# Kernel optimization log

Hardware: AMD Instinct MI355X
Metric: run time of the kernel (lower is better)

Reference implementation:

```python
import jax, jax.numpy as jnp
import numpy as np
from jax import lax

EPS = 1e-8

def _norm(v, eps=EPS):
    # matches torch F.normalize: v / max(||v||, eps)
    return v / jnp.maximum(jnp.linalg.norm(v, axis=-1, keepdims=True), eps)

def keep_r6(r6):
    v1 = _norm(r6[..., :3])
    v2 = r6[..., 3:6]
    v2 = v2 - jnp.sum(v2 * v1, axis=-1, keepdims=True) * v1
    v2n = jnp.linalg.norm(v2, axis=-1, keepdims=True)
    mask = (v2n < 1e-6).astype(r6.dtype)
    e1 = jnp.array([1.0, 0.0, 0.0], dtype=r6.dtype)
    e2 = jnp.array([0.0, 1.0, 0.0], dtype=r6.dtype)
    dot = jnp.abs(jnp.sum(v1 * e1, axis=-1, keepdims=True))
    fb = jnp.where(dot < 0.9, e1, e2)
    fb_v2 = jnp.cross(v1, jnp.broadcast_to(fb, v1.shape), axis=-1)
    v2 = (1.0 - mask) * v2 + mask * fb_v2
    v2 = _norm(v2)
    return jnp.concatenate([v1, v2], axis=-1)

def r6_to_matrix(r6):
    r6 = keep_r6(r6)
    v1, v2 = r6[..., :3], r6[..., 3:6]
    v3 = jnp.cross(v1, v2, axis=-1)
    R = jnp.stack([v1, v2, v3], axis=-1)  # columns v1,v2,v3
    det = jnp.linalg.det(R)
    return R * jnp.sign(det)[..., None, None]

def instance_norm(x, eps=1e-5):
    # InstanceNorm3d, affine=False: per-(B,C) stats over spatial dims, biased var
    mu = jnp.mean(x, axis=(2, 3, 4), keepdims=True)
    var = jnp.mean((x - mu) ** 2, axis=(2, 3, 4), keepdims=True)
    return (x - mu) * lax.rsqrt(var + eps)

def conv1x1(x, w, b):
    return jnp.einsum('oc,bcdhw->bodhw', w[:, :, 0, 0, 0], x) + b[None, :, None, None, None]

def conv3_circ(x, w, b):
    xp = jnp.pad(x, ((0, 0), (0, 0), (1, 1), (1, 1), (1, 1)), mode='wrap')
    out = lax.conv_general_dilated(xp, w, (1, 1, 1), 'VALID',
                                   dimension_numbers=('NCDHW', 'OIDHW', 'NCDHW'))
    return out + b[None, :, None, None, None]

def _gelu(t):
    return jax.nn.gelu(t, approximate=False)

def _forward(x, pos_emb, qkv_w, qkv_b, lp1_w, lp1_b, lp2_w, lp2_b,
             mod1_w, mod1_b, mod2_w, mod2_b, pa_w, pa_b,
             R6_d, R6_h, R6_w, proj_w, proj_b):
    B, C, D, H, W = x.shape
    NH = pa_w.shape[0]
    HD = C // NH
    NV = HD // 3
    scale = HD ** (-0.5)

    # PositionalProcessing (deterministic; computed once, reused for all 3 axes)
    local = conv1x1(_gelu(instance_norm(conv3_circ(pos_emb, lp1_w, lp1_b))), lp2_w, lp2_b)
    mod = jax.nn.sigmoid(conv1x1(_gelu(instance_norm(conv1x1(local, mod1_w, mod1_b))), mod2_w, mod2_b))
    x_mod = x * mod
    pos_attn = _gelu(instance_norm(conv1x1(pos_emb, pa_w, pa_b)))  # [B,NH,D,H,W]

    axes = [
        (R6_d, (0, 3, 4, 1, 2), (0, 4, 3, 1, 2)),  # depth
        (R6_h, (0, 2, 4, 1, 3), (0, 4, 1, 3, 2)),  # height
        (R6_w, (0, 2, 3, 1, 4), (0, 4, 1, 2, 3)),  # width
    ]
    out_sum = 0.0
    for R6, perm, inv in axes:
        xp = jnp.transpose(x_mod, perm)      # [B, A1, A2, C, L]
        Bb, A1, A2, _, L = xp.shape
        bd = Bb * A1 * A2
        xl = jnp.swapaxes(xp.reshape(bd, C, L), -1, -2)  # [bd, L, C]
        qkv = (xl @ qkv_w.T + qkv_b).reshape(bd, L, 3, NH, HD)
        qkv = jnp.transpose(qkv, (2, 0, 3, 1, 4))
        q, k, v = qkv[0], qkv[1], qkv[2]     # [bd, NH, L, HD]
        R = r6_to_matrix(keep_r6(R6))[0]     # [NH, 3, 3]

        def rot(t):
            tv = t.reshape(bd, NH, L, NV, 3)
            return jnp.einsum('hij,bhlvj->bhlvi', R, tv).reshape(bd, NH, L, HD)

        attn = jnp.einsum('bhqd,bhkd->bhqk', rot(q), rot(k)) * scale
        pa = jnp.transpose(pos_attn, perm).reshape(bd, NH, L)
        attn = jax.nn.softmax(attn + pa[..., None], axis=-1)
        o = jnp.einsum('bhqk,bhkd->bhqd', attn, v)      # [bd, NH, L, HD]
        o = jnp.swapaxes(o, 1, 2).reshape(Bb, A1, A2, L, C)
        out_sum = out_sum + jnp.transpose(o, inv)        # [B, C, D, H, W]
    return conv1x1(out_sum, proj_w, proj_b)


def setup_inputs() -> dict:
    key = jax.random.key(0)
    ks = jax.random.split(key, 20)
    B, C, D, H, W, NH = 2, 96, 40, 40, 40, 4

    def rn(k, shape, s=0.05):
        return jax.random.normal(k, shape, dtype=jnp.float32) * s

    return {
        'x': jax.random.normal(ks[0], (B, C, D, H, W), dtype=jnp.float32),
        'pos_emb': jax.random.normal(ks[1], (B, C, D, H, W), dtype=jnp.float32),
        'qkv_w': rn(ks[2], (3 * C, C)), 'qkv_b': rn(ks[3], (3 * C,)),
        'lp1_w': rn(ks[4], (C, C, 3, 3, 3)), 'lp1_b': rn(ks[5], (C,)),
        'lp2_w': rn(ks[6], (C, C, 1, 1, 1)), 'lp2_b': rn(ks[7], (C,)),
        'mod1_w': rn(ks[8], (C, C, 1, 1, 1)), 'mod1_b': rn(ks[9], (C,)),
        'mod2_w': rn(ks[10], (C, C, 1, 1, 1)), 'mod2_b': rn(ks[11], (C,)),
        'pa_w': rn(ks[12], (NH, C, 1, 1, 1)), 'pa_b': rn(ks[13], (NH,)),
        'R6_d': jax.random.normal(ks[14], (1, NH, 6), dtype=jnp.float32),
        'R6_h': jax.random.normal(ks[15], (1, NH, 6), dtype=jnp.float32),
        'R6_w': jax.random.normal(ks[16], (1, NH, 6), dtype=jnp.float32),
        'proj_w': rn(ks[17], (C, C, 1, 1, 1)), 'proj_b': rn(ks[18], (C,)),
    }


def reference(x, pos_emb, qkv_w, qkv_b, lp1_w, lp1_b, lp2_w, lp2_b,
              mod1_w, mod1_b, mod2_w, mod2_b, pa_w, pa_b,
              R6_d, R6_h, R6_w, proj_w, proj_b):
    return _forward(x, pos_emb, qkv_w, qkv_b, lp1_w, lp1_b, lp2_w, lp2_b,
                    mod1_w, mod1_b, mod2_w, mod2_b, pa_w, pa_b,
                    R6_d, R6_h, R6_w, proj_w, proj_b)
```

## Files before the change

### kernel.cpp

```cpp
#include <hip/hip_runtime.h>


typedef __attribute__((ext_vector_type(8))) _Float16 half8;
typedef __attribute__((ext_vector_type(2))) _Float16 half2;
typedef __attribute__((ext_vector_type(16))) float floatx16;

static __device__ __forceinline__ half2 h2(unsigned int u) {
    return __builtin_bit_cast(half2, u);
}
static __device__ __forceinline__ float fdot2(unsigned int a, unsigned int b, float c) {
    return __builtin_amdgcn_fdot2(h2(a), h2(b), c, false);
}

__global__ void k_zero(float* __restrict__ p) {
    int t = threadIdx.x;
    for (int i = t; i < 768; i += 256) p[i] = 0.f;
}

__global__ __launch_bounds__(256) void k_cvt_in(const float* __restrict__ pos,
                                                _Float16* __restrict__ in_t) {
    __shared__ _Float16 lds[64][97];
    int bid = blockIdx.x;
    int b = bid / 1000, s0 = (bid % 1000) * 64;
    int t = threadIdx.x;
    for (int i = t; i < 6144; i += 256) {
        int c = i / 64, sl = i % 64;
        lds[sl][c] = (_Float16)pos[(b * 96 + c) * 64000 + s0 + sl];
    }
    __syncthreads();
    _Float16* outp = in_t + ((size_t)b * 64000 + s0) * 96;
    for (int i = t; i < 6144; i += 256) {
        int sl = i / 96, c = i % 96;
        outp[i] = lds[sl][c];
    }
}

__global__ void k_cvt_w(const float* __restrict__ w, _Float16* __restrict__ wf) {
    int i = blockIdx.x * 256 + threadIdx.x;
    if (i < 248832) {
        int c = i % 96, m = (i / 96) % 96, tap = i / 9216;
        wf[i] = (_Float16)w[(m * 96 + c) * 27 + tap];
    }
}

__global__ void k_cvt_f16(const float* __restrict__ w, _Float16* __restrict__ o, int n) {
    int i = blockIdx.x * 256 + threadIdx.x;
    if (i < n) o[i] = (_Float16)w[i];
}

__global__ __launch_bounds__(256) void k_fold(const float* __restrict__ lp2_w,
                                              const float* __restrict__ lp2_b,
                                              const float* __restrict__ mod1_w,
                                              const float* __restrict__ mod1_b,
                                              _Float16* __restrict__ wfold,
                                              float* __restrict__ bfold) {
    int i = blockIdx.x * 256 + threadIdx.x;
    if (i < 9216) {
        int o = i / 96, c = i % 96;
        float a = 0.f;
        for (int k = 0; k < 96; k++) a += mod1_w[o * 96 + k] * lp2_w[k * 96 + c];
        wfold[i] = (_Float16)a;
    }
    if (blockIdx.x == 0 && threadIdx.x < 96) {
        int o = threadIdx.x;
        float a = mod1_b[o];
        for (int k = 0; k < 96; k++) a += mod1_w[o * 96 + k] * lp2_b[k];
        bfold[o] = a;
    }
}

__global__ __launch_bounds__(256) void k_conv3_v2(const _Float16* __restrict__ in_t,
                                                  const _Float16* __restrict__ wf,
                                                  const float* __restrict__ bias,
                                                  _Float16* __restrict__ c3) {
    __shared__ int tbl[27 * 256];
    __shared__ _Float16 st[256 * 98];
    __shared__ float bsh[96];
    int t = threadIdx.x;
    int bid = blockIdx.x;
    {
        int xcd = bid & 7, idx = bid >> 3;
        bid = (xcd < 4) ? (xcd * 63 + idx) : (252 + (xcd - 4) * 62 + idx);
    }
    int b = bid / 250;
    int s0 = (bid % 250) * 256;

    for (int u = t; u < 27 * 256; u += 256) {
        int tap = u >> 8, nl = u & 255;
        int kd = tap / 9, kh = (tap / 3) % 3, kw = tap % 3;
        int s = s0 + nl;
        int d = s / 1600, r = s - d * 1600;
        int h = r / 40, w = r - h * 40;
        int ds = d + kd - 1; if (ds < 0) ds += 40; else if (ds >= 40) ds -= 40;
        int hs = h + kh - 1; if (hs < 0) hs += 40; else if (hs >= 40) hs -= 40;
        int wv2 = w + kw - 1; if (wv2 < 0) wv2 += 40; else if (wv2 >= 40) wv2 -= 40;
        tbl[u] = ((ds * 1600 + hs * 40 + wv2) * 96) * 2;
    }
    if (t < 96) bsh[t] = bias[t];
    __syncthreads();

    int wv = t >> 6, lane = t & 63;
    int n31 = lane & 31, kg = lane >> 5;
    const char* inb = (const char*)(in_t + (size_t)b * 64000 * 96) + kg * 16;

    floatx16 acc[3][2];
#pragma unroll
    for (int mt = 0; mt < 3; mt++)
#pragma unroll
        for (int nt = 0; nt < 2; nt++)
#pragma unroll
            for (int r = 0; r < 16; r++) acc[mt][nt][r] = 0.f;

    for (int tap = 0; tap < 27; tap++) {
        int ta0 = tbl[tap * 256 + wv * 64 + n31];
        int ta1 = tbl[tap * 256 + wv * 64 + 32 + n31];
        const char* pb0 = inb + ta0;
        const char* pb1 = inb + ta1;
        const _Float16* wt = wf + tap * 9216 + kg * 8;
#pragma unroll
        for (int j = 0; j < 6; j++) {
            half8 a0 = *(const half8*)(wt + (n31) * 96 + j * 16);
            half8 a1 = *(const half8*)(wt + (32 + n31) * 96 + j * 16);
            half8 a2 = *(const half8*)(wt + (64 + n31) * 96 + j * 16);
            half8 b0 = *(const half8*)(pb0 + j * 32);
            half8 b1 = *(const half8*)(pb1 + j * 32);
            acc[0][0] = __builtin_amdgcn_mfma_f32_32x32x16_f16(a0, b0, acc[0][0], 0, 0, 0);
            acc[0][1] = __builtin_amdgcn_mfma_f32_32x32x16_f16(a0, b1, acc[0][1], 0, 0, 0);
            acc[1][0] = __builtin_amdgcn_mfma_f32_32x32x16_f16(a1, b0, acc[1][0], 0, 0, 0);
            acc[1][1] = __builtin_amdgcn_mfma_f32_32x32x16_f16(a1, b1, acc[1][1], 0, 0, 0);
            acc[2][0] = __builtin_amdgcn_mfma_f32_32x32x16_f16(a2, b0, acc[2][0], 0, 0, 0);
            acc[2][1] = __builtin_amdgcn_mfma_f32_32x32x16_f16(a2, b1, acc[2][1], 0, 0, 0);
        }
    }

#pragma unroll
    for (int mt = 0; mt < 3; mt++)
#pragma unroll
        for (int nt = 0; nt < 2; nt++)
#pragma unroll
            for (int r = 0; r < 16; r++) {
                int m = mt * 32 + (r & 3) + 8 * (r >> 2) + 4 * kg;
                int sl = wv * 64 + nt * 32 + n31;
                st[sl * 98 + m] = (_Float16)(acc[mt][nt][r] + bsh[m]);
            }
    __syncthreads();

    unsigned int* dst = (unsigned int*)(c3 + ((size_t)(b * 64000 + s0)) * 96);
    for (int i = t; i < 12288; i += 256) {
        int row = i / 48, sg = i % 48;
        __builtin_nontemporal_store(*(const unsigned int*)&st[row * 98 + sg * 2], &dst[i]);
    }
}

__global__ __launch_bounds__(192) void k_stats_sc(const _Float16* __restrict__ in,
                                                  float* __restrict__ raw) {
    __shared__ float red_s[16][96], red_q[16][96];
    int bid = blockIdx.x;
    int b = bid / 50, ch = bid % 50;
    int t = threadIdx.x;
    int sp = t / 12, cs = t % 12;
    const uint4* base = (const uint4*)(in + ((size_t)(b * 64000 + ch * 1280)) * 96);
    float s8[8], q8[8];
#pragma unroll
    for (int e = 0; e < 8; e++) { s8[e] = 0.f; q8[e] = 0.f; }
    for (int i = 0; i < 80; i++) {
        uint4 v = base[(sp + i * 16) * 12 + cs];
        half8 h = __builtin_bit_cast(half8, v);
#pragma unroll
        for (int e = 0; e < 8; e++) { float f = (float)h[e]; s8[e] += f; q8[e] += f * f; }
    }
#pragma unroll
    for (int e = 0; e < 8; e++) { red_s[sp][cs * 8 + e] = s8[e]; red_q[sp][cs * 8 + e] = q8[e]; }
    __syncthreads();
    if (t < 96) {
        float S = 0.f, Q = 0.f;
        for (int k = 0; k < 16; k++) { S += red_s[k][t]; Q += red_q[k][t]; }
        atomicAdd(&raw[(b * 96 + t) * 2], S);
        atomicAdd(&raw[(b * 96 + t) * 2 + 1], Q);
    }
}

__global__ void k_finalize(const float* __restrict__ raw, float2* __restrict__ sf) {
    int t = threadIdx.x;
    if (t < 192) {
        float S = raw[t * 2], Q = raw[t * 2 + 1];
        float mu = S * (1.f / 64000.f);
        float var = Q * (1.f / 64000.f) - mu * mu;
        sf[t] = make_float2(mu, rsqrtf(var + 1e-5f));
    }
}

__global__ __launch_bounds__(256) void k_ng16(_Float16* __restrict__ x, const float2* __restrict__ sf) {
    int t = threadIdx.x, bid = blockIdx.x;
    uint4* p = (uint4*)x;
#pragma unroll
    for (int k = 0; k < 4; k++) {
        int i = bid * 1024 + k * 256 + t;
        int e0 = i * 8;
        int b = e0 / 6144000;
        int c0 = e0 % 96;
        const float2* sp = &sf[b * 96 + c0];
        uint4 v = p[i];
        half8 h = __builtin_bit_cast(half8, v);
        _Float16 o[8];
#pragma unroll
        for (int e = 0; e < 8; e++) {
            float2 st = sp[e];
            float u = ((float)h[e] - st.x) * st.y;
            o[e] = (_Float16)(0.5f * u * (1.f + erff(u * 0.70710678118654752f)));
        }
        p[i] = *(uint4*)o;
    }
}

template <int MODE>
__global__ __launch_bounds__(256) void k_gemm96(const _Float16* __restrict__ in,
                                                const _Float16* __restrict__ w,
                                                const float* __restrict__ bias,
                                                const float* __restrict__ xg,
                                                _Float16* __restrict__ outp) {
    __shared__ _Float16 un[12544];
    __shared__ float bias_s[96];
    int t = threadIdx.x, bid = blockIdx.x;
    int b = bid / 500, s0 = (bid % 500) * 128;
    for (int i = t; i < 1152; i += 256) ((uint4*)un)[i] = ((const uint4*)w)[i];
    if (t < 96) bias_s[t] = bias[t];
    __syncthreads();

    int ws = t >> 6, lane = t & 63;
    int n = lane & 31, kg = lane >> 5;
    int p = ws * 32 + n;
    const uint4* brow = (const uint4*)(in + ((size_t)(b * 64000 + s0 + p)) * 96);
    uint4 bf[6];
#pragma unroll
    for (int kc = 0; kc < 6; kc++) bf[kc] = brow[kc * 2 + kg];

    floatx16 acc[3];
#pragma unroll
    for (int mt = 0; mt < 3; mt++)
#pragma unroll
        for (int r = 0; r < 16; r++) acc[mt][r] = 0.f;
#pragma unroll
    for (int kc = 0; kc < 6; kc++) {
        half8 bfh = __builtin_bit_cast(half8, bf[kc]);
#pragma unroll
        for (int mt = 0; mt < 3; mt++) {
            uint4 au = *(const uint4*)&un[(mt * 32 + n) * 96 + kc * 16 + kg * 8];
            acc[mt] = __builtin_amdgcn_mfma_f32_32x32x16_f16(__builtin_bit_cast(half8, au), bfh, acc[mt], 0, 0, 0);
        }
    }
    __syncthreads();

#pragma unroll
    for (int mt = 0; mt < 3; mt++)
#pragma unroll
        for (int r = 0; r < 16; r++) {
            int m = mt * 32 + (r & 3) + 8 * (r >> 2) + 4 * kg;
            int sl = ws * 32 + n;
            float v = acc[mt][r] + bias_s[m];
            if (MODE == 1) {
                v = 1.f / (1.f + __expf(-v));
                v *= xg[((size_t)(b * 96 + m)) * 64000 + s0 + sl];
            }
            un[sl * 98 + m] = (_Float16)v;
        }
    __syncthreads();

    unsigned int* dst = (unsigned int*)(outp + ((size_t)(b * 64000 + s0)) * 96);
    for (int i = t; i < 6144; i += 256) {
        int row = i / 48, sg = i % 48;
        dst[i] = *(const unsigned int*)&un[row * 98 + sg * 2];
    }
}

__global__ __launch_bounds__(256) void k_qkv(const _Float16* __restrict__ xt,
                                             const _Float16* __restrict__ wq,
                                             const float* __restrict__ qb,
                                             _Float16* __restrict__ qA) {
    __shared__ _Float16 smem[27648];
    __shared__ float bias_s[288];
    int t = threadIdx.x;
    int bid = blockIdx.x;
    int b = bid / 500;
    int s0 = (bid % 500) * 128;

    for (int i = t; i < 3456; i += 256) ((uint4*)smem)[i] = ((const uint4*)wq)[i];
    for (int i = t; i < 288; i += 256) bias_s[i] = qb[i];
    __syncthreads();

    int ws = t >> 6, lane = t & 63;
    int n = lane & 31, kg = lane >> 5;
    int p = ws * 32 + n;

    const uint4* brow = (const uint4*)(xt + ((size_t)(b * 64000 + s0 + p)) * 96);
    uint4 bf[6];
#pragma unroll
    for (int kc = 0; kc < 6; kc++) bf[kc] = brow[kc * 2 + kg];

    floatx16 acc[9];
#pragma unroll
    for (int mt = 0; mt < 9; mt++)
#pragma unroll
        for (int r = 0; r < 16; r++) acc[mt][r] = 0.f;

#pragma unroll
    for (int kc = 0; kc < 6; kc++) {
        half8 bfh = __builtin_bit_cast(half8, bf[kc]);
#pragma unroll
        for (int mt = 0; mt < 9; mt++) {
            uint4 au = *(const uint4*)&smem[(mt * 32 + n) * 96 + kc * 16 + kg * 8];
            acc[mt] = __builtin_amdgcn_mfma_f32_32x32x16_f16(__builtin_bit_cast(half8, au), bfh, acc[mt], 0, 0, 0);
        }
    }

    const float scale = 0.20412414523193154f;
    for (int q = 0; q < 2; q++) {
        __syncthreads();
        if ((ws >> 1) == q) {
            int pl = (ws & 1) * 32 + n;
#pragma unroll
            for (int mt = 0; mt < 9; mt++)
#pragma unroll
                for (int g = 0; g < 4; g++) {
                    int m0 = mt * 32 + g * 8 + kg * 4;
                    _Float16 tm[4];
#pragma unroll
                    for (int j = 0; j < 4; j++) {
                        float v = acc[mt][g * 4 + j] + bias_s[m0 + j];
                        if (m0 + j < 96) v *= scale;
                        tm[j] = (_Float16)v;
                    }
                    *(uint2*)&smem[pl * 296 + m0] = *(uint2*)tm;
                }
        }
        __syncthreads();
        for (int idx = t; idx < 2304; idx += 256) {
            int pl = idx / 36, seg = idx % 36;
            int s = s0 + q * 64 + pl;
            uint4 v = *(const uint4*)&smem[pl * 296 + seg * 8];
            *(uint4*)&qA[((size_t)(b * 64000 + s)) * 288 + seg * 8] = v;
        }
    }
}

template <int AXIS, bool ACC>
__global__ __launch_bounds__(320, 3) void k_attn(const _Float16* __restrict__ qA,
                                                 _Float16* __restrict__ osum) {
    __shared__ _Float16 kk[8352];
    __shared__ _Float16 vT[7744];
    int t = threadIdx.x;
    int bid = blockIdx.x;
    int b = bid / 800;
    int r0 = (bid % 800) * 2;

    auto smap = [&](int r, int l) -> int {
        if (AXIS == 0) return l * 1600 + r;
        else if (AXIS == 1) { int d = r / 40, w = r % 40; return d * 1600 + l * 40 + w; }
        else return r * 40 + l;
    };
    const uint4* src = (const uint4*)qA;
    for (int i = t; i < 960; i += 320) {
        int line = i / 480, key = (i % 480) / 12, seg = i % 12;
        int row = b * 64000 + smap(r0 + line, key);
        ((uint4*)kk)[i] = src[(size_t)row * 36 + 12 + seg];
    }
    for (int i = t; i < 960; i += 320) {
        int line = i / 480, key = (i % 480) / 12, seg = i % 12;
        int row = b * 64000 + smap(r0 + line, key);
        uint4 v = src[(size_t)row * 36 + 24 + seg];
        _Float16 tmp[8];
        *(uint4*)tmp = v;
#pragma unroll
        for (int e = 0; e < 8; e++) {
            int hdg = seg * 8 + e;
            vT[(line * 4 + hdg / 24) * 968 + (hdg % 24) * 40 + key] = tmp[e];
        }
    }

    int line = t / 160, head = (t % 160) / 40, ql = t % 40;
    int rr = r0 + line;
    unsigned int qu[12];
    {
        const uint4* qp = (const uint4*)(qA + ((size_t)(b * 64000 + smap(rr, ql))) * 288 + head * 24);
#pragma unroll
        for (int j = 0; j < 3; j++) *(uint4*)&qu[j * 4] = qp[j];
    }
    __syncthreads();

    float s[40];
    const uint4* kbase = (const uint4*)kk + line * 480 + head * 3;
#pragma unroll 4
    for (int key = 0; key < 40; key++) {
        unsigned int kku[12];
#pragma unroll
        for (int j = 0; j < 3; j++) *(uint4*)&kku[j * 4] = kbase[key * 12 + j];
        float a = 0.f;
#pragma unroll
        for (int i = 0; i < 12; i++) a = fdot2(kku[i], qu[i], a);
        s[key] = a;
    }

    float mx = -1e30f;
#pragma unroll
    for (int i = 0; i < 40; i++) mx = fmaxf(mx, s[i]);
    float sum = 0.f;
#pragma unroll
    for (int i = 0; i < 40; i++) { s[i] = __expf(s[i] - mx); sum += s[i]; }
    float inv = 1.f / sum;

    unsigned int pw[20];
#pragma unroll
    for (int i = 0; i < 20; i++) {
        half2 a = { (_Float16)(s[2 * i] * inv), (_Float16)(s[2 * i + 1] * inv) };
        pw[i] = __builtin_bit_cast(unsigned int, a);
    }

    __syncthreads();

    float o[24];
    const uint4* vbase = (const uint4*)vT + (line * 4 + head) * 121;
#pragma unroll 2
    for (int hd = 0; hd < 24; hd++) {
        unsigned int vv[20];
#pragma unroll
        for (int j = 0; j < 5; j++) *(uint4*)&vv[j * 4] = vbase[hd * 5 + j];
        float a = 0.f;
#pragma unroll
        for (int i = 0; i < 20; i++) a = fdot2(vv[i], pw[i], a);
        o[hd] = a;
    }

    {
        _Float16 tm[24];
#pragma unroll
        for (int j = 0; j < 24; j++) tm[j] = (_Float16)o[j];
        _Float16* dA = &kk[(line * 40 + ql) * 104 + head * 24];
#pragma unroll
        for (int j = 0; j < 3; j++) ((uint4*)dA)[j] = ((uint4*)tm)[j];
    }
    __syncthreads();

    uint4* dst = (uint4*)osum;
    for (int i = t; i < 960; i += 320) {
        int row = i / 12, seg = i % 12;
        int s2 = smap(r0 + row / 40, row % 40);
        size_t di = ((size_t)(b * 64000 + s2)) * 12 + seg;
        uint4 v = *(const uint4*)&kk[row * 104 + seg * 8];
        if (ACC) {
            half8 a = __builtin_bit_cast(half8, dst[di]);
            half8 c = __builtin_bit_cast(half8, v);
            dst[di] = __builtin_bit_cast(uint4, a + c);
        } else {
            dst[di] = v;
        }
    }
}

__global__ __launch_bounds__(256) void k_proj(const _Float16* __restrict__ osum,
                                              const _Float16* __restrict__ wp,
                                              const float* __restrict__ pb,
                                              float* __restrict__ out) {
    __shared__ _Float16 A[9216];
    __shared__ float bias_s[96];
    int t = threadIdx.x;
    int bid = blockIdx.x;
    int b = bid / 500;
    int s0 = (bid % 500) * 128;
    for (int i = t; i < 1152; i += 256) ((uint4*)A)[i] = ((const uint4*)wp)[i];
    if (t < 96) bias_s[t] = pb[t];
    __syncthreads();

    int ws = t >> 6, lane = t & 63;
    int n = lane & 31, kg = lane >> 5;
    int s = s0 + ws * 32 + n;

    const uint4* brow = (const uint4*)(osum + ((size_t)(b * 64000 + s0 + ws * 32 + n)) * 96);
    uint4 bf[6];
#pragma unroll
    for (int kc = 0; kc < 6; kc++) bf[kc] = brow[kc * 2 + kg];

    floatx16 acc[3];
#pragma unroll
    for (int mt = 0; mt < 3; mt++)
#pragma unroll
        for (int r = 0; r < 16; r++) acc[mt][r] = 0.f;

#pragma unroll
    for (int kc = 0; kc < 6; kc++) {
        half8 bfh = __builtin_bit_cast(half8, bf[kc]);
#pragma unroll
        for (int mt = 0; mt < 3; mt++) {
            uint4 au = *(const uint4*)&A[(mt * 32 + n) * 96 + kc * 16 + kg * 8];
            acc[mt] = __builtin_amdgcn_mfma_f32_32x32x16_f16(__builtin_bit_cast(half8, au), bfh, acc[mt], 0, 0, 0);
        }
    }

#pragma unroll
    for (int mt = 0; mt < 3; mt++)
#pragma unroll
        for (int r = 0; r < 16; r++) {
            int m = mt * 32 + (r & 3) + 8 * (r >> 2) + 4 * kg;
            out[((size_t)(b * 96 + m)) * 64000 + s] = acc[mt][r] + bias_s[m];
        }
}

extern "C" void kernel_launch(void* const* d_in, const int* in_sizes, int n_in,
                              void* d_out, int out_size, void* d_ws, size_t ws_size,
                              hipStream_t stream) {
    const float* x      = (const float*)d_in[0];
    const float* pos    = (const float*)d_in[1];
    const float* qkv_w  = (const float*)d_in[2];
    const float* qkv_b  = (const float*)d_in[3];
    const float* lp1_w  = (const float*)d_in[4];
    const float* lp1_b  = (const float*)d_in[5];
    const float* lp2_w  = (const float*)d_in[6];
    const float* lp2_b  = (const float*)d_in[7];
    const float* mod1_w = (const float*)d_in[8];
    const float* mod1_b = (const float*)d_in[9];
    const float* mod2_w = (const float*)d_in[10];
    const float* mod2_b = (const float*)d_in[11];
    const float* proj_w = (const float*)d_in[17];
    const float* proj_b = (const float*)d_in[18];
    float* out = (float*)d_out;
    float* ws = (float*)d_ws;

    _Float16* bufA = (_Float16*)ws;
    _Float16* bufB = (_Float16*)(ws + 6144000);
    _Float16* qA   = (_Float16*)(ws + 12288000);
    _Float16* in_t = qA;
    _Float16* wf   = (_Float16*)(ws + 30720000);
    _Float16* wq   = (_Float16*)(ws + 30844416);
    _Float16* wpj  = (_Float16*)(ws + 30858240);
    _Float16* wfold= (_Float16*)(ws + 30862848);
    _Float16* wm2  = (_Float16*)(ws + 30867456);
    float* bfold   = ws + 30872064;
    float* raw     = ws + 30872160;
    float2* sf0    = (float2*)(ws + 30872928);
    float2* sf1    = (float2*)(ws + 30873312);
    float* raw0 = raw, *raw1 = raw + 384;

    k_zero<<<1, 256, 0, stream>>>(raw);
    k_cvt_in<<<2000, 256, 0, stream>>>(pos, in_t);
    k_cvt_w<<<972, 256, 0, stream>>>(lp1_w, wf);
    k_fold<<<36, 256, 0, stream>>>(lp2_w, lp2_b, mod1_w, mod1_b, wfold, bfold);
    k_cvt_f16<<<36, 256, 0, stream>>>(mod2_w, wm2, 9216);
    k_cvt_f16<<<108, 256, 0, stream>>>(qkv_w, wq, 27648);
    k_cvt_f16<<<36, 256, 0, stream>>>(proj_w, wpj, 9216);

    k_conv3_v2<<<500, 256, 0, stream>>>(in_t, wf, lp1_b, bufA);
    k_stats_sc<<<100, 192, 0, stream>>>(bufA, raw0);
    k_finalize<<<1, 256, 0, stream>>>(raw0, sf0);
    k_ng16<<<1500, 256, 0, stream>>>(bufA, sf0);
    k_gemm96<0><<<1000, 256, 0, stream>>>(bufA, wfold, bfold, nullptr, bufB);
    k_stats_sc<<<100, 192, 0, stream>>>(bufB, raw1);
    k_finalize<<<1, 256, 0, stream>>>(raw1, sf1);
    k_ng16<<<1500, 256, 0, stream>>>(bufB, sf1);
    k_gemm96<1><<<1000, 256, 0, stream>>>(bufB, wm2, mod2_b, x, bufA);

    k_qkv<<<1000, 256, 0, stream>>>(bufA, wq, qkv_b, qA);
    k_attn<2, false><<<1600, 320, 0, stream>>>(qA, bufB);
    k_attn<0, true ><<<1600, 320, 0, stream>>>(qA, bufB);
    k_attn<1, true ><<<1600, 320, 0, stream>>>(qA, bufB);

    k_proj<<<1000, 256, 0, stream>>>(bufB, wpj, proj_b, out);
}
```

Baseline: 687.0 us.

## Fuse instance-norm stats and GELU into conv3 and gemm96 epilogues/prologues

Removes the separate stats, normalize-GELU passes and their extra full-tensor read/write. Per-channel sum and sum-of-squares are now accumulated from the LDS tile in the conv3 and gemm96<0> epilogues, and normalize+GELU is applied to the gemm96 input fragments in registers. The conv3 kernel is also retiled to 128 spatial points per block with registers-only wrap addressing (no LDS tap table) and an XCD-aware block remap, with a matching remap in the input transpose. Tradeoffs: more atomics contention, a serial 128-row reduction loop by 96 threads, and halved per-wave B reuse in conv3.

```diff
diff --git a/kernel.cpp b/kernel.cpp
--- a/kernel.cpp
+++ b/kernel.cpp
@@ -21,7 +21,10 @@
                                                 _Float16* __restrict__ in_t) {
     __shared__ _Float16 lds[64][97];
     int bid = blockIdx.x;
-    int b = bid / 1000, s0 = (bid % 1000) * 64;
+    int xcd = bid & 7, idx = bid >> 3;
+    int L = xcd * 125 + (idx >> 1);
+    int b = L / 500;
+    int s0 = (L % 500) * 128 + (idx & 1) * 64;
     int t = threadIdx.x;
     for (int i = t; i < 6144; i += 256) {
         int c = i / 64, sl = i % 64;
@@ -69,114 +72,78 @@
     }
 }
 
-__global__ __launch_bounds__(256) void k_conv3_v2(const _Float16* __restrict__ in_t,
-                                                  const _Float16* __restrict__ wf,
-                                                  const float* __restrict__ bias,
-                                                  _Float16* __restrict__ c3) {
-    __shared__ int tbl[27 * 256];
-    __shared__ _Float16 st[256 * 98];
+__global__ __launch_bounds__(256, 4) void k_conv3_v3(const _Float16* __restrict__ in_t,
+                                                     const _Float16* __restrict__ wf,
+                                                     const float* __restrict__ bias,
+                                                     _Float16* __restrict__ c3,
+                                                     float* __restrict__ raw0) {
+    __shared__ _Float16 st[128 * 98];
     __shared__ float bsh[96];
     int t = threadIdx.x;
     int bid = blockIdx.x;
-    {
-        int xcd = bid & 7, idx = bid >> 3;
-        bid = (xcd < 4) ? (xcd * 63 + idx) : (252 + (xcd - 4) * 62 + idx);
-    }
-    int b = bid / 250;
-    int s0 = (bid % 250) * 256;
-
-    for (int u = t; u < 27 * 256; u += 256) {
-        int tap = u >> 8, nl = u & 255;
-        int kd = tap / 9, kh = (tap / 3) % 3, kw = tap % 3;
-        int s = s0 + nl;
-        int d = s / 1600, r = s - d * 1600;
-        int h = r / 40, w = r - h * 40;
-        int ds = d + kd - 1; if (ds < 0) ds += 40; else if (ds >= 40) ds -= 40;
-        int hs = h + kh - 1; if (hs < 0) hs += 40; else if (hs >= 40) hs -= 40;
-        int wv2 = w + kw - 1; if (wv2 < 0) wv2 += 40; else if (wv2 >= 40) wv2 -= 40;
-        tbl[u] = ((ds * 1600 + hs * 40 + wv2) * 96) * 2;
-    }
+    { int xcd = bid & 7; bid = xcd * 125 + (bid >> 3); }
+    int b = bid / 500, s0 = (bid % 500) * 128;
+
     if (t < 96) bsh[t] = bias[t];
-    __syncthreads();
 
     int wv = t >> 6, lane = t & 63;
     int n31 = lane & 31, kg = lane >> 5;
     const char* inb = (const char*)(in_t + (size_t)b * 64000 * 96) + kg * 16;
 
-    floatx16 acc[3][2];
+    int s = s0 + wv * 32 + n31;
+    int d = s / 1600, r = s - d * 1600;
+    int h = r / 40, w = r - h * 40;
+    int Ad[3] = { (d == 0 ? 39 : d - 1) * 307200, d * 307200, (d == 39 ? 0 : d + 1) * 307200 };
+    int Ah[3] = { (h == 0 ? 39 : h - 1) * 7680,   h * 7680,   (h == 39 ? 0 : h + 1) * 7680 };
+    int Aw[3] = { (w == 0 ? 39 : w - 1) * 192,    w * 192,    (w == 39 ? 0 : w + 1) * 192 };
+
+    floatx16 acc[3];
 #pragma unroll
     for (int mt = 0; mt < 3; mt++)
 #pragma unroll
-        for (int nt = 0; nt < 2; nt++)
-#pragma unroll
-            for (int r = 0; r < 16; r++) acc[mt][nt][r] = 0.f;
-
+        for (int r2 = 0; r2 < 16; r2++) acc[mt][r2] = 0.f;
+
+#pragma unroll
     for (int tap = 0; tap < 27; tap++) {
-        int ta0 = tbl[tap * 256 + wv * 64 + n31];
-        int ta1 = tbl[tap * 256 + wv * 64 + 32 + n31];
-        const char* pb0 = inb + ta0;
-        const char* pb1 = inb + ta1;
+        const int kd = tap / 9, kh = (tap / 3) % 3, kw = tap % 3;
+        const char* pb = inb + (Ad[kd] + Ah[kh] + Aw[kw]);
         const _Float16* wt = wf + tap * 9216 + kg * 8;
 #pragma unroll
         for (int j = 0; j < 6; j++) {
-            half8 a0 = *(const half8*)(wt + (n31) * 96 + j * 16);
+            half8 b0 = *(const half8*)(pb + j * 32);
+            half8 a0 = *(const half8*)(wt + n31 * 96 + j * 16);
             half8 a1 = *(const half8*)(wt + (32 + n31) * 96 + j * 16);
             half8 a2 = *(const half8*)(wt + (64 + n31) * 96 + j * 16);
-            half8 b0 = *(const half8*)(pb0 + j * 32);
-            half8 b1 = *(const half8*)(pb1 + j * 32);
-            acc[0][0] = __builtin_amdgcn_mfma_f32_32x32x16_f16(a0, b0, acc[0][0], 0, 0, 0);
-            acc[0][1] = __builtin_amdgcn_mfma_f32_32x32x16_f16(a0, b1, acc[0][1], 0, 0, 0);
-            acc[1][0] = __builtin_amdgcn_mfma_f32_32x32x16_f16(a1, b0, acc[1][0], 0, 0, 0);
-            acc[1][1] = __builtin_amdgcn_mfma_f32_32x32x16_f16(a1, b1, acc[1][1], 0, 0, 0);
-            acc[2][0] = __builtin_amdgcn_mfma_f32_32x32x16_f16(a2, b0, acc[2][0], 0, 0, 0);
-            acc[2][1] = __builtin_amdgcn_mfma_f32_32x32x16_f16(a2, b1, acc[2][1], 0, 0, 0);
-        }
-    }
-
+            acc[0] = __builtin_amdgcn_mfma_f32_32x32x16_f16(a0, b0, acc[0], 0, 0, 0);
+            acc[1] = __builtin_amdgcn_mfma_f32_32x32x16_f16(a1, b0, acc[1], 0, 0, 0);
+            acc[2] = __builtin_amdgcn_mfma_f32_32x32x16_f16(a2, b0, acc[2], 0, 0, 0);
+        }
+    }
+
+    __syncthreads();
 #pragma unroll
     for (int mt = 0; mt < 3; mt++)
 #pragma unroll
-        for (int nt = 0; nt < 2; nt++)
-#pragma unroll
-            for (int r = 0; r < 16; r++) {
-                int m = mt * 32 + (r & 3) + 8 * (r >> 2) + 4 * kg;
-                int sl = wv * 64 + nt * 32 + n31;
-                st[sl * 98 + m] = (_Float16)(acc[mt][nt][r] + bsh[m]);
-            }
+        for (int r2 = 0; r2 < 16; r2++) {
+            int m = mt * 32 + (r2 & 3) + 8 * (r2 >> 2) + 4 * kg;
+            int sl = wv * 32 + n31;
+            st[sl * 98 + m] = (_Float16)(acc[mt][r2] + bsh[m]);
+        }
     __syncthreads();
 
     unsigned int* dst = (unsigned int*)(c3 + ((size_t)(b * 64000 + s0)) * 96);
-    for (int i = t; i < 12288; i += 256) {
+    for (int i = t; i < 6144; i += 256) {
         int row = i / 48, sg = i % 48;
         __builtin_nontemporal_store(*(const unsigned int*)&st[row * 98 + sg * 2], &dst[i]);
     }
-}
-
-__global__ __launch_bounds__(192) void k_stats_sc(const _Float16* __restrict__ in,
-                                                  float* __restrict__ raw) {
-    __shared__ float red_s[16][96], red_q[16][96];
-    int bid = blockIdx.x;
-    int b = bid / 50, ch = bid % 50;
-    int t = threadIdx.x;
-    int sp = t / 12, cs = t % 12;
-    const uint4* base = (const uint4*)(in + ((size_t)(b * 64000 + ch * 1280)) * 96);
-    float s8[8], q8[8];
-#pragma unroll
-    for (int e = 0; e < 8; e++) { s8[e] = 0.f; q8[e] = 0.f; }
-    for (int i = 0; i < 80; i++) {
-        uint4 v = base[(sp + i * 16) * 12 + cs];
-        half8 h = __builtin_bit_cast(half8, v);
-#pragma unroll
-        for (int e = 0; e < 8; e++) { float f = (float)h[e]; s8[e] += f; q8[e] += f * f; }
-    }
-#pragma unroll
-    for (int e = 0; e < 8; e++) { red_s[sp][cs * 8 + e] = s8[e]; red_q[sp][cs * 8 + e] = q8[e]; }
-    __syncthreads();
     if (t < 96) {
         float S = 0.f, Q = 0.f;
-        for (int k = 0; k < 16; k++) { S += red_s[k][t]; Q += red_q[k][t]; }
-        atomicAdd(&raw[(b * 96 + t) * 2], S);
-        atomicAdd(&raw[(b * 96 + t) * 2 + 1], Q);
+        for (int r2 = 0; r2 < 128; r2++) {
+            float f = (float)st[r2 * 98 + t];
+            S += f; Q += f * f;
+        }
+        atomicAdd(&raw0[(b * 96 + t) * 2], S);
+        atomicAdd(&raw0[(b * 96 + t) * 2 + 1], Q);
     }
 }
 
@@ -190,41 +157,21 @@
     }
 }
 
-__global__ __launch_bounds__(256) void k_ng16(_Float16* __restrict__ x, const float2* __restrict__ sf) {
-    int t = threadIdx.x, bid = blockIdx.x;
-    uint4* p = (uint4*)x;
-#pragma unroll
-    for (int k = 0; k < 4; k++) {
-        int i = bid * 1024 + k * 256 + t;
-        int e0 = i * 8;
-        int b = e0 / 6144000;
-        int c0 = e0 % 96;
-        const float2* sp = &sf[b * 96 + c0];
-        uint4 v = p[i];
-        half8 h = __builtin_bit_cast(half8, v);
-        _Float16 o[8];
-#pragma unroll
-        for (int e = 0; e < 8; e++) {
-            float2 st = sp[e];
-            float u = ((float)h[e] - st.x) * st.y;
-            o[e] = (_Float16)(0.5f * u * (1.f + erff(u * 0.70710678118654752f)));
-        }
-        p[i] = *(uint4*)o;
-    }
-}
-
 template <int MODE>
 __global__ __launch_bounds__(256) void k_gemm96(const _Float16* __restrict__ in,
                                                 const _Float16* __restrict__ w,
                                                 const float* __restrict__ bias,
+                                                const float2* __restrict__ sf,
                                                 const float* __restrict__ xg,
+                                                float* __restrict__ rawout,
                                                 _Float16* __restrict__ outp) {
     __shared__ _Float16 un[12544];
     __shared__ float bias_s[96];
+    __shared__ float2 sfs[96];
     int t = threadIdx.x, bid = blockIdx.x;
     int b = bid / 500, s0 = (bid % 500) * 128;
     for (int i = t; i < 1152; i += 256) ((uint4*)un)[i] = ((const uint4*)w)[i];
-    if (t < 96) bias_s[t] = bias[t];
+    if (t < 96) { bias_s[t] = bias[t]; sfs[t] = sf[b * 96 + t]; }
     __syncthreads();
 
     int ws = t >> 6, lane = t & 63;
@@ -234,6 +181,19 @@
     uint4 bf[6];
 #pragma unroll
     for (int kc = 0; kc < 6; kc++) bf[kc] = brow[kc * 2 + kg];
+
+#pragma unroll
+    for (int kc = 0; kc < 6; kc++) {
+        half8 hv = __builtin_bit_cast(half8, bf[kc]);
+        _Float16 o[8];
+#pragma unroll
+        for (int e = 0; e < 8; e++) {
+            float2 s2 = sfs[kc * 16 + kg * 8 + e];
+            float u = ((float)hv[e] - s2.x) * s2.y;
+            o[e] = (_Float16)(0.5f * u * (1.f + erff(u * 0.70710678118654752f)));
+        }
+        bf[kc] = *(const uint4*)o;
+    }
 
     floatx16 acc[3];
 #pragma unroll
@@ -265,6 +225,16 @@
             un[sl * 98 + m] = (_Float16)v;
         }
     __syncthreads();
+
+    if (MODE == 0 && t < 96) {
+        float S = 0.f, Q = 0.f;
+        for (int r2 = 0; r2 < 128; r2++) {
+            float f = (float)un[r2 * 98 + t];
+            S += f; Q += f * f;
+        }
+        atomicAdd(&rawout[(b * 96 + t) * 2], S);
+        atomicAdd(&rawout[(b * 96 + t) * 2 + 1], Q);
+    }
 
     unsigned int* dst = (unsigned int*)(outp + ((size_t)(b * 64000 + s0)) * 96);
     for (int i = t; i < 6144; i += 256) {
@@ -547,15 +517,11 @@
     k_cvt_f16<<<108, 256, 0, stream>>>(qkv_w, wq, 27648);
     k_cvt_f16<<<36, 256, 0, stream>>>(proj_w, wpj, 9216);
 
-    k_conv3_v2<<<500, 256, 0, stream>>>(in_t, wf, lp1_b, bufA);
-    k_stats_sc<<<100, 192, 0, stream>>>(bufA, raw0);
+    k_conv3_v3<<<1000, 256, 0, stream>>>(in_t, wf, lp1_b, bufA, raw0);
     k_finalize<<<1, 256, 0, stream>>>(raw0, sf0);
-    k_ng16<<<1500, 256, 0, stream>>>(bufA, sf0);
-    k_gemm96<0><<<1000, 256, 0, stream>>>(bufA, wfold, bfold, nullptr, bufB);
-    k_stats_sc<<<100, 192, 0, stream>>>(bufB, raw1);
+    k_gemm96<0><<<1000, 256, 0, stream>>>(bufA, wfold, bfold, sf0, nullptr, raw1, bufB);
     k_finalize<<<1, 256, 0, stream>>>(raw1, sf1);
-    k_ng16<<<1500, 256, 0, stream>>>(bufB, sf1);
-    k_gemm96<1><<<1000, 256, 0, stream>>>(bufB, wm2, mod2_b, x, bufA);
+    k_gemm96<1><<<1000, 256, 0, stream>>>(bufB, wm2, mod2_b, sf1, x, nullptr, bufA);
 
     k_qkv<<<1000, 256, 0, stream>>>(bufA, wq, qkv_b, qA);
     k_attn<2, false><<<1600, 320, 0, stream>>>(qA, bufB);
```

New measurement: 843.3 us. 22.7% more time.
